# Kernel optimization log

Measured on AMD Instinct MI355X. Metric: run time of the kernel, lower is better.

Reference implementation:

```python
import jax, jax.numpy as jnp
import numpy as np

B, TQ, TK = 4, 256, 256
Q, K, H = 256, 256, 256


def setup_inputs() -> dict:
    key = jax.random.key(0)
    ks = jax.random.split(key, 10)
    s = 0.05
    return {
        "queries": jax.random.normal(ks[0], (B, TQ, Q), dtype=jnp.float32),
        "keys": jax.random.normal(ks[1], (B, TK, K), dtype=jnp.float32),
        # lengths in [T//2, T] so no fully-masked query rows (torch would NaN there too)
        "query_lengths": jax.random.randint(ks[2], (B,), TQ // 2, TQ + 1),
        "key_lengths": jax.random.randint(ks[3], (B,), TK // 2, TK + 1),
        # nn.Linear(Q+K, H): weight applied as x @ W1; torch concat order is [keys, queries]
        "W1": jax.random.normal(ks[4], (K + Q, H), dtype=jnp.float32) * s,
        "b1": jax.random.normal(ks[5], (H,), dtype=jnp.float32) * s,
        "W2": jax.random.normal(ks[6], (H, H), dtype=jnp.float32) * s,
        "b2": jax.random.normal(ks[7], (H,), dtype=jnp.float32) * s,
        "W3": jax.random.normal(ks[8], (H, 1), dtype=jnp.float32) * s,
        "b3": jax.random.normal(ks[9], (1,), dtype=jnp.float32) * s,
    }


def reference(queries, keys, query_lengths, key_lengths, W1, b1, W2, b2, W3, b3):
    Bn, Tq, Qd = queries.shape
    Tk, Kd = keys.shape[1], keys.shape[2]
    # Split the first linear: concat([keys, queries]) @ W1 == keys@W1[:K] + queries@W1[K:]
    kh = jnp.einsum("bkd,dh->bkh", keys, W1[:Kd])      # [B,Tk,H]
    qh = jnp.einsum("bqd,dh->bqh", queries, W1[Kd:])   # [B,Tq,H]
    h = jax.nn.relu(qh[:, :, None, :] + kh[:, None, :, :] + b1)  # [B,Tq,Tk,H]
    h = jax.nn.relu(jnp.einsum("bqkh,hg->bqkg", h, W2) + b2)     # [B,Tq,Tk,H]
    scores = jnp.einsum("bqkh,h->bqk", h, W3[:, 0]) + b3[0]       # [B,Tq,Tk]
    # mask True where position is padding (query OR key out of range)
    mask = (jnp.arange(Tq)[None, :, None] >= query_lengths[:, None, None]) | (
        jnp.arange(Tk)[None, None, :] >= key_lengths[:, None, None]
    )
    scores = jnp.where(mask, -1e30, scores)
    probs = jax.nn.softmax(scores, axis=-1)
    probs = jnp.where(mask, 0.0, probs)
    return jnp.einsum("bqk,bkd->bqd", probs, keys)  # [B,Tq,K]
```

## Files before the change

### kernel.cpp

```cpp
#include <hip/hip_runtime.h>
#include <cstdint>

#define BATCH 4
#define TQ 256
#define TK 256
#define DIM 256
#define HD 256

typedef _Float16 f16x8 __attribute__((ext_vector_type(8)));
typedef float f32x4 __attribute__((ext_vector_type(4)));

union U4H8 { uint4 u; f16x8 v; };

#define KEEP(x) asm volatile("" : "+v"(x))

__device__ __forceinline__ unsigned short f2h(float f) {
    _Float16 h = (_Float16)f;
    unsigned short u;
    __builtin_memcpy(&u, &h, 2);
    return u;
}

__device__ __forceinline__ uint32_t pk2h(float a, float b) {
    auto r = __builtin_amdgcn_cvt_pkrtz(a, b);
    uint32_t w;
    __builtin_memcpy(&w, &r, 4);
    return w;
}

__global__ __launch_bounds__(256) void prep_all(
    const float* __restrict__ queries, const float* __restrict__ keys,
    const float* __restrict__ W1, const float* __restrict__ b1,
    const float* __restrict__ W2,
    float* __restrict__ qh, float* __restrict__ kh,
    unsigned short* __restrict__ W2T) {
    int i = blockIdx.x;
    int t = threadIdx.x;
    if (i >= 256) {
        __shared__ float tile[32][33];
        int bi = i - 256;
        int tx = t & 31, ty = t >> 5;
        int tc = (bi & 7) * 32, tn = (bi >> 3) * 32;
#pragma unroll
        for (int r = 0; r < 4; ++r)
            tile[ty + r * 8][tx] = W2[(tc + ty + r * 8) * HD + tn + tx];
        __syncthreads();
#pragma unroll
        for (int r = 0; r < 4; ++r)
            W2T[(tn + ty + r * 8) * HD + tc + tx] = f2h(tile[tx][ty + r * 8]);
        return;
    }
    bool isQ = i < 128;
    int r0 = (i & 127) * 8;
    const float* X = isQ ? queries : keys;
    const float* W = W1 + (isQ ? DIM * HD : 0);
    float* O = isQ ? qh : kh;
    __shared__ float xs[8][DIM];
#pragma unroll
    for (int r = 0; r < 8; ++r) xs[r][t] = X[(r0 + r) * DIM + t];
    __syncthreads();
    float acc[8] = {0.f, 0.f, 0.f, 0.f, 0.f, 0.f, 0.f, 0.f};
#pragma unroll 8
    for (int d = 0; d < DIM; ++d) {
        float w = W[d * HD + t];
#pragma unroll
        for (int r = 0; r < 8; ++r) acc[r] = fmaf(xs[r][d], w, acc[r]);
    }
    float bias = isQ ? b1[t] : 0.f;
#pragma unroll
    for (int r = 0; r < 8; ++r) O[(r0 + r) * HD + t] = acc[r] + bias;
}

__global__ __launch_bounds__(256, 2) void mlp_attn(
    const float* __restrict__ qh, const float* __restrict__ kh,
    const unsigned short* __restrict__ W2T,
    const float* __restrict__ b2, const float* __restrict__ W3,
    const float* __restrict__ keys,
    const int* __restrict__ qlens, const int* __restrict__ klens,
    float* __restrict__ out) {
    int bid = blockIdx.x;
    int b = bid >> 8;
    int q = bid & 255;
    int t = threadIdx.x;
    float* orow = out + (b * TQ + q) * DIM;
    if (q >= qlens[b]) { orow[t] = 0.f; return; }
    int klen = klens[b];
    int nch = (klen + 63) >> 6;

    __shared__ uint4 Afrag[2][8][4][64];
    __shared__ float srow[TK];
    __shared__ float red[8];

    int wid = t >> 6, lane = t & 63;
    int col = lane & 15, quad = lane >> 4;

    int nb = wid * 64;
    uint4 bfr[4][8];
    float b2v[4], w3v[4];
#pragma unroll
    for (int nt = 0; nt < 4; ++nt) {
        int n = nb + nt * 16 + col;
        const uint4* r = (const uint4*)(W2T + n * HD) + quad;
#pragma unroll
        for (int s = 0; s < 8; ++s) bfr[nt][s] = r[s * 4];
        b2v[nt] = b2[n];
        w3v[nt] = W3[n];
    }

    int p = t >> 2, j8 = t & 3;
    const float* qrow = qh + (b * TQ + q) * HD + j8 * 8;
    const float* kbase = kh + b * TK * HD + j8 * 8;
    int aoff = ((p >> 4) << 6) | (p & 15) | (j8 << 4);

    auto stage = [&](int c, int d) {
        const float* krow = kbase + (c * 64 + p) * HD;
        uint4* aslot = &Afrag[d][0][0][0] + aoff;
#pragma unroll 2
        for (int s = 0; s < 8; ++s) {
            const float4 k0 = *(const float4*)(krow + s * 32);
            const float4 k1 = *(const float4*)(krow + s * 32 + 4);
            const float4 q0 = *(const float4*)(qrow + s * 32);
            const float4 q1 = *(const float4*)(qrow + s * 32 + 4);
            uint4 w;
            w.x = pk2h(fmaxf(k0.x + q0.x, 0.f), fmaxf(k0.y + q0.y, 0.f));
            w.y = pk2h(fmaxf(k0.z + q0.z, 0.f), fmaxf(k0.w + q0.w, 0.f));
            w.z = pk2h(fmaxf(k1.x + q1.x, 0.f), fmaxf(k1.y + q1.y, 0.f));
            w.w = pk2h(fmaxf(k1.z + q1.z, 0.f), fmaxf(k1.w + q1.w, 0.f));
            aslot[s * 256] = w;
        }
    };

    srow[t] = 0.f;
    stage(0, 0);

#pragma unroll
    for (int nt = 0; nt < 4; ++nt)
#pragma unroll
        for (int s = 0; s < 8; ++s) {
            KEEP(bfr[nt][s].x); KEEP(bfr[nt][s].y);
            KEEP(bfr[nt][s].z); KEEP(bfr[nt][s].w);
        }

    __syncthreads();

    for (int c = 0; c < nch; ++c) {
        int cur = c & 1;
        if (c + 1 < nch) stage(c + 1, cur ^ 1);

        f32x4 acc[4][4] = {};
#pragma unroll
        for (int s = 0; s < 8; ++s) {
#pragma unroll
            for (int mt = 0; mt < 4; ++mt) {
                U4H8 au;
                au.u = Afrag[cur][s][mt][lane];
#pragma unroll
                for (int nt = 0; nt < 4; ++nt) {
                    U4H8 bu;
                    bu.u = bfr[nt][s];
                    acc[mt][nt] = __builtin_amdgcn_mfma_f32_16x16x32_f16(
                        au.v, bu.v, acc[mt][nt], 0, 0, 0);
                }
            }
        }

#pragma unroll
        for (int mt = 0; mt < 4; ++mt) {
            float part[4];
#pragma unroll
            for (int r = 0; r < 4; ++r) {
                float pa = 0.f;
#pragma unroll
                for (int nt = 0; nt < 4; ++nt)
                    pa = fmaf(fmaxf(acc[mt][nt][r] + b2v[nt], 0.f), w3v[nt], pa);
                part[r] = pa;
            }
#pragma unroll
            for (int off = 1; off < 16; off <<= 1)
#pragma unroll
                for (int r = 0; r < 4; ++r)
                    part[r] += __shfl_xor(part[r], off, 64);
            if (col == 0)
#pragma unroll
                for (int r = 0; r < 4; ++r)
                    atomicAdd(&srow[c * 64 + mt * 16 + quad * 4 + r], part[r]);
        }
        __syncthreads();
    }

    float s = (t < klen) ? srow[t] : -3.4e38f;
    float m = s;
#pragma unroll
    for (int off = 1; off < 64; off <<= 1) m = fmaxf(m, __shfl_xor(m, off, 64));
    if (lane == 0) red[wid] = m;
    __syncthreads();
    m = fmaxf(fmaxf(red[0], red[1]), fmaxf(red[2], red[3]));
    float e = (t < klen) ? __expf(s - m) : 0.f;
    float sum = e;
#pragma unroll
    for (int off = 1; off < 64; off <<= 1) sum += __shfl_xor(sum, off, 64);
    if (lane == 0) red[4 + wid] = sum;
    __syncthreads();
    float denom = red[4] + red[5] + red[6] + red[7];
    srow[t] = e / denom;
    __syncthreads();

    float acc = 0.f;
    const float* kp = keys + b * TK * DIM + t;
#pragma unroll 8
    for (int k = 0; k < klen; ++k) acc = fmaf(srow[k], kp[k * DIM], acc);
    orow[t] = acc;
}

extern "C" void kernel_launch(void* const* d_in, const int* in_sizes, int n_in,
                              void* d_out, int out_size, void* d_ws, size_t ws_size,
                              hipStream_t stream) {
    (void)in_sizes; (void)n_in; (void)out_size; (void)ws_size;
    const float* queries = (const float*)d_in[0];
    const float* keys    = (const float*)d_in[1];
    const int*   qlens   = (const int*)d_in[2];
    const int*   klens   = (const int*)d_in[3];
    const float* W1      = (const float*)d_in[4];
    const float* b1      = (const float*)d_in[5];
    const float* W2      = (const float*)d_in[6];
    const float* b2      = (const float*)d_in[7];
    const float* W3      = (const float*)d_in[8];
    float* out = (float*)d_out;

    float* qh = (float*)d_ws;
    float* kh = qh + BATCH * TQ * HD;
    unsigned short* W2T = (unsigned short*)(kh + BATCH * TK * HD);

    prep_all<<<320, 256, 0, stream>>>(queries, keys, W1, b1, W2, qh, kh, W2T);
    mlp_attn<<<BATCH * TQ, 256, 0, stream>>>(
        qh, kh, W2T, b2, W3, keys, qlens, klens, out);
}
```

Baseline: 148.8 us.

## Process two queries per block with interleaved staging and XCD-aware block swizzle

Each mlp_attn block now handles two adjacent query rows over 32-key chunks, so the W2 fragments held in registers and the final keys pass are shared across two queries. Staging of the next chunk is split into register prefetch of kh and conversion interleaved with the MFMA loop to overlap loads with compute. Block indices are remapped across groups of 8, likely to spread work across XCDs, and prep_all uses 4 rows per block for more parallelism. Costs include more registers, and fewer blocks (512) which may reduce latency hiding; padding queries in a pair still do full work.

```diff
diff --git a/kernel.cpp b/kernel.cpp
--- a/kernel.cpp
+++ b/kernel.cpp
@@ -36,9 +36,9 @@
     unsigned short* __restrict__ W2T) {
     int i = blockIdx.x;
     int t = threadIdx.x;
-    if (i >= 256) {
+    if (i >= 512) {
         __shared__ float tile[32][33];
-        int bi = i - 256;
+        int bi = i - 512;
         int tx = t & 31, ty = t >> 5;
         int tc = (bi & 7) * 32, tn = (bi >> 3) * 32;
 #pragma unroll
@@ -50,25 +50,25 @@
             W2T[(tn + ty + r * 8) * HD + tc + tx] = f2h(tile[tx][ty + r * 8]);
         return;
     }
-    bool isQ = i < 128;
-    int r0 = (i & 127) * 8;
+    bool isQ = i < 256;
+    int r0 = (i & 255) * 4;
     const float* X = isQ ? queries : keys;
     const float* W = W1 + (isQ ? DIM * HD : 0);
     float* O = isQ ? qh : kh;
-    __shared__ float xs[8][DIM];
-#pragma unroll
-    for (int r = 0; r < 8; ++r) xs[r][t] = X[(r0 + r) * DIM + t];
-    __syncthreads();
-    float acc[8] = {0.f, 0.f, 0.f, 0.f, 0.f, 0.f, 0.f, 0.f};
+    __shared__ float xs[4][DIM];
+#pragma unroll
+    for (int r = 0; r < 4; ++r) xs[r][t] = X[(r0 + r) * DIM + t];
+    __syncthreads();
+    float acc[4] = {0.f, 0.f, 0.f, 0.f};
 #pragma unroll 8
     for (int d = 0; d < DIM; ++d) {
         float w = W[d * HD + t];
 #pragma unroll
-        for (int r = 0; r < 8; ++r) acc[r] = fmaf(xs[r][d], w, acc[r]);
+        for (int r = 0; r < 4; ++r) acc[r] = fmaf(xs[r][d], w, acc[r]);
     }
     float bias = isQ ? b1[t] : 0.f;
 #pragma unroll
-    for (int r = 0; r < 8; ++r) O[(r0 + r) * HD + t] = acc[r] + bias;
+    for (int r = 0; r < 4; ++r) O[(r0 + r) * HD + t] = acc[r] + bias;
 }
 
 __global__ __launch_bounds__(256, 2) void mlp_attn(
@@ -78,28 +78,31 @@
     const float* __restrict__ keys,
     const int* __restrict__ qlens, const int* __restrict__ klens,
     float* __restrict__ out) {
-    int bid = blockIdx.x;
-    int b = bid >> 8;
-    int q = bid & 255;
+    int orig = blockIdx.x;
+    int bid = ((orig & 7) << 6) | (orig >> 3);
+    int b = bid >> 7;
+    int q0 = (bid & 127) << 1;
     int t = threadIdx.x;
-    float* orow = out + (b * TQ + q) * DIM;
-    if (q >= qlens[b]) { orow[t] = 0.f; return; }
+    int qlen = qlens[b];
+    float* orow = out + (b * TQ + q0) * DIM;
+    if (q0 >= qlen) { orow[t] = 0.f; orow[DIM + t] = 0.f; return; }
+    bool v1 = (q0 + 1) < qlen;
     int klen = klens[b];
-    int nch = (klen + 63) >> 6;
+    int nch = (klen + 31) >> 5;
 
     __shared__ uint4 Afrag[2][8][4][64];
-    __shared__ float srow[TK];
-    __shared__ float red[8];
-
-    int wid = t >> 6, lane = t & 63;
+    __shared__ float srow[2][TK];
+    __shared__ float red[16];
+
+    int w = t >> 6, lane = t & 63;
     int col = lane & 15, quad = lane >> 4;
 
-    int nb = wid * 64;
+    int nb = w << 6;
     uint4 bfr[4][8];
     float b2v[4], w3v[4];
 #pragma unroll
     for (int nt = 0; nt < 4; ++nt) {
-        int n = nb + nt * 16 + col;
+        int n = nb + (nt << 4) + col;
         const uint4* r = (const uint4*)(W2T + n * HD) + quad;
 #pragma unroll
         for (int s = 0; s < 8; ++s) bfr[nt][s] = r[s * 4];
@@ -107,31 +110,30 @@
         w3v[nt] = W3[n];
     }
 
-    int p = t >> 2, j8 = t & 3;
-    const float* qrow = qh + (b * TQ + q) * HD + j8 * 8;
-    const float* kbase = kh + b * TK * HD + j8 * 8;
-    int aoff = ((p >> 4) << 6) | (p & 15) | (j8 << 4);
-
-    auto stage = [&](int c, int d) {
-        const float* krow = kbase + (c * 64 + p) * HD;
-        uint4* aslot = &Afrag[d][0][0][0] + aoff;
+    int qsel = w >> 1;
+    int rsub = ((w & 1) << 4) | col;
+    const float* qrow = qh + (b * TQ + q0 + qsel) * HD + (quad << 3);
+    const float* kbase = kh + b * TK * HD + (quad << 3);
+
+    {
+        const float* krow = kbase + rsub * HD;
+        uint4* as = &Afrag[0][0][w][lane];
 #pragma unroll 2
         for (int s = 0; s < 8; ++s) {
             const float4 k0 = *(const float4*)(krow + s * 32);
             const float4 k1 = *(const float4*)(krow + s * 32 + 4);
-            const float4 q0 = *(const float4*)(qrow + s * 32);
-            const float4 q1 = *(const float4*)(qrow + s * 32 + 4);
-            uint4 w;
-            w.x = pk2h(fmaxf(k0.x + q0.x, 0.f), fmaxf(k0.y + q0.y, 0.f));
-            w.y = pk2h(fmaxf(k0.z + q0.z, 0.f), fmaxf(k0.w + q0.w, 0.f));
-            w.z = pk2h(fmaxf(k1.x + q1.x, 0.f), fmaxf(k1.y + q1.y, 0.f));
-            w.w = pk2h(fmaxf(k1.z + q1.z, 0.f), fmaxf(k1.w + q1.w, 0.f));
-            aslot[s * 256] = w;
-        }
-    };
-
-    srow[t] = 0.f;
-    stage(0, 0);
+            const float4 qa = *(const float4*)(qrow + s * 32);
+            const float4 qb = *(const float4*)(qrow + s * 32 + 4);
+            uint4 wv;
+            wv.x = pk2h(fmaxf(k0.x + qa.x, 0.f), fmaxf(k0.y + qa.y, 0.f));
+            wv.y = pk2h(fmaxf(k0.z + qa.z, 0.f), fmaxf(k0.w + qa.w, 0.f));
+            wv.z = pk2h(fmaxf(k1.x + qb.x, 0.f), fmaxf(k1.y + qb.y, 0.f));
+            wv.w = pk2h(fmaxf(k1.z + qb.z, 0.f), fmaxf(k1.w + qb.w, 0.f));
+            as[s * 256] = wv;
+        }
+    }
+    srow[0][t] = 0.f;
+    srow[1][t] = 0.f;
 
 #pragma unroll
     for (int nt = 0; nt < 4; ++nt)
@@ -145,71 +147,115 @@
 
     for (int c = 0; c < nch; ++c) {
         int cur = c & 1;
-        if (c + 1 < nch) stage(c + 1, cur ^ 1);
-
-        f32x4 acc[4][4] = {};
-#pragma unroll
-        for (int s = 0; s < 8; ++s) {
-#pragma unroll
-            for (int mt = 0; mt < 4; ++mt) {
-                U4H8 au;
-                au.u = Afrag[cur][s][mt][lane];
-#pragma unroll
-                for (int nt = 0; nt < 4; ++nt) {
-                    U4H8 bu;
-                    bu.u = bfr[nt][s];
-                    acc[mt][nt] = __builtin_amdgcn_mfma_f32_16x16x32_f16(
-                        au.v, bu.v, acc[mt][nt], 0, 0, 0);
+        bool stg = (c + 1 < nch);
+        const float* krow = kbase + (((c + 1) << 5) + rsub) * HD;
+        uint4* as = &Afrag[cur ^ 1][0][w][lane];
+        float4 Rk0[4], Rk1[4];
+        if (stg) {
+#pragma unroll
+            for (int p = 0; p < 4; ++p) {
+                Rk0[p] = *(const float4*)(krow + p * 32);
+                Rk1[p] = *(const float4*)(krow + p * 32 + 4);
+            }
+        }
+
+#pragma unroll
+        for (int hf = 0; hf < 2; ++hf) {
+            f32x4 acc[2][4] = {};
+#pragma unroll
+            for (int s = 0; s < 8; ++s) {
+#pragma unroll
+                for (int m2 = 0; m2 < 2; ++m2) {
+                    U4H8 au;
+                    au.u = Afrag[cur][s][(hf << 1) | m2][lane];
+#pragma unroll
+                    for (int nt = 0; nt < 4; ++nt) {
+                        U4H8 bu;
+                        bu.u = bfr[nt][s];
+                        acc[m2][nt] = __builtin_amdgcn_mfma_f32_16x16x32_f16(
+                            au.v, bu.v, acc[m2][nt], 0, 0, 0);
+                    }
+                }
+                if (hf == 0 && stg) {
+                    int rp = s & 3;
+                    const float4 qa = *(const float4*)(qrow + s * 32);
+                    const float4 qb = *(const float4*)(qrow + s * 32 + 4);
+                    uint4 wv;
+                    wv.x = pk2h(fmaxf(Rk0[rp].x + qa.x, 0.f), fmaxf(Rk0[rp].y + qa.y, 0.f));
+                    wv.y = pk2h(fmaxf(Rk0[rp].z + qa.z, 0.f), fmaxf(Rk0[rp].w + qa.w, 0.f));
+                    wv.z = pk2h(fmaxf(Rk1[rp].x + qb.x, 0.f), fmaxf(Rk1[rp].y + qb.y, 0.f));
+                    wv.w = pk2h(fmaxf(Rk1[rp].z + qb.z, 0.f), fmaxf(Rk1[rp].w + qb.w, 0.f));
+                    as[s * 256] = wv;
+                    if (s < 4) {
+                        Rk0[rp] = *(const float4*)(krow + (s + 4) * 32);
+                        Rk1[rp] = *(const float4*)(krow + (s + 4) * 32 + 4);
+                    }
                 }
             }
-        }
-
-#pragma unroll
-        for (int mt = 0; mt < 4; ++mt) {
-            float part[4];
-#pragma unroll
-            for (int r = 0; r < 4; ++r) {
-                float pa = 0.f;
-#pragma unroll
-                for (int nt = 0; nt < 4; ++nt)
-                    pa = fmaf(fmaxf(acc[mt][nt][r] + b2v[nt], 0.f), w3v[nt], pa);
-                part[r] = pa;
+#pragma unroll
+            for (int m2 = 0; m2 < 2; ++m2) {
+                float part[4];
+#pragma unroll
+                for (int r = 0; r < 4; ++r) {
+                    float pa = 0.f;
+#pragma unroll
+                    for (int nt = 0; nt < 4; ++nt)
+                        pa = fmaf(fmaxf(acc[m2][nt][r] + b2v[nt], 0.f), w3v[nt], pa);
+                    part[r] = pa;
+                }
+#pragma unroll
+                for (int off = 1; off < 16; off <<= 1)
+#pragma unroll
+                    for (int r = 0; r < 4; ++r)
+                        part[r] += __shfl_xor(part[r], off, 64);
+                if (col == 0)
+#pragma unroll
+                    for (int r = 0; r < 4; ++r)
+                        atomicAdd(&srow[hf][(c << 5) | (m2 << 4) | (quad << 2) | r],
+                                  part[r]);
             }
-#pragma unroll
-            for (int off = 1; off < 16; off <<= 1)
-#pragma unroll
-                for (int r = 0; r < 4; ++r)
-                    part[r] += __shfl_xor(part[r], off, 64);
-            if (col == 0)
-#pragma unroll
-                for (int r = 0; r < 4; ++r)
-                    atomicAdd(&srow[c * 64 + mt * 16 + quad * 4 + r], part[r]);
         }
         __syncthreads();
     }
 
-    float s = (t < klen) ? srow[t] : -3.4e38f;
-    float m = s;
-#pragma unroll
-    for (int off = 1; off < 64; off <<= 1) m = fmaxf(m, __shfl_xor(m, off, 64));
-    if (lane == 0) red[wid] = m;
-    __syncthreads();
-    m = fmaxf(fmaxf(red[0], red[1]), fmaxf(red[2], red[3]));
-    float e = (t < klen) ? __expf(s - m) : 0.f;
-    float sum = e;
-#pragma unroll
-    for (int off = 1; off < 64; off <<= 1) sum += __shfl_xor(sum, off, 64);
-    if (lane == 0) red[4 + wid] = sum;
-    __syncthreads();
-    float denom = red[4] + red[5] + red[6] + red[7];
-    srow[t] = e / denom;
-    __syncthreads();
-
-    float acc = 0.f;
+    float s0 = (t < klen) ? srow[0][t] : -3.4e38f;
+    float s1 = (t < klen) ? srow[1][t] : -3.4e38f;
+    float m0 = s0, m1 = s1;
+#pragma unroll
+    for (int off = 1; off < 64; off <<= 1) {
+        m0 = fmaxf(m0, __shfl_xor(m0, off, 64));
+        m1 = fmaxf(m1, __shfl_xor(m1, off, 64));
+    }
+    if (lane == 0) { red[w] = m0; red[8 + w] = m1; }
+    __syncthreads();
+    m0 = fmaxf(fmaxf(red[0], red[1]), fmaxf(red[2], red[3]));
+    m1 = fmaxf(fmaxf(red[8], red[9]), fmaxf(red[10], red[11]));
+    float e0 = (t < klen) ? __expf(s0 - m0) : 0.f;
+    float e1 = (t < klen) ? __expf(s1 - m1) : 0.f;
+    float u0 = e0, u1 = e1;
+#pragma unroll
+    for (int off = 1; off < 64; off <<= 1) {
+        u0 += __shfl_xor(u0, off, 64);
+        u1 += __shfl_xor(u1, off, 64);
+    }
+    if (lane == 0) { red[4 + w] = u0; red[12 + w] = u1; }
+    __syncthreads();
+    float d0 = red[4] + red[5] + red[6] + red[7];
+    float d1 = red[12] + red[13] + red[14] + red[15];
+    srow[0][t] = e0 / d0;
+    srow[1][t] = e1 / d1;
+    __syncthreads();
+
+    float a0 = 0.f, a1 = 0.f;
     const float* kp = keys + b * TK * DIM + t;
 #pragma unroll 8
-    for (int k = 0; k < klen; ++k) acc = fmaf(srow[k], kp[k * DIM], acc);
-    orow[t] = acc;
+    for (int k = 0; k < klen; ++k) {
+        float v = kp[k * DIM];
+        a0 = fmaf(srow[0][k], v, a0);
+        a1 = fmaf(srow[1][k], v, a1);
+    }
+    orow[t] = a0;
+    orow[DIM + t] = v1 ? a1 : 0.f;
 }
 
 extern "C" void kernel_launch(void* const* d_in, const int* in_sizes, int n_in,
@@ -231,7 +277,7 @@
     float* kh = qh + BATCH * TQ * HD;
     unsigned short* W2T = (unsigned short*)(kh + BATCH * TK * HD);
 
-    prep_all<<<320, 256, 0, stream>>>(queries, keys, W1, b1, W2, qh, kh, W2T);
-    mlp_attn<<<BATCH * TQ, 256, 0, stream>>>(
+    prep_all<<<576, 256, 0, stream>>>(queries, keys, W1, b1, W2, qh, kh, W2T);
+    mlp_attn<<<BATCH * TQ / 2, 256, 0, stream>>>(
         qh, kh, W2T, b2, W3, keys, qlens, klens, out);
 }
```

Result: no change. 149.3 us (+0.3%).
